# Kernel optimization log

Hardware: AMD Instinct MI355X
Metric: run time of the kernel (lower is better)

The kernel has to match this reference:

```python
import jax, jax.numpy as jnp
import numpy as np
import math

B, S, E, H = 4, 2048, 1024, 16
D = E // H
INFINITY = 1000000.0

def setup_inputs() -> dict:
    key = jax.random.key(0)
    ks = jax.random.split(key, 10)
    std = 1.0 / math.sqrt(E)
    inp = {
        "x": jax.random.normal(ks[0], (B, S, E), dtype=jnp.float32),
        "mask": jax.random.randint(ks[1], (B, S), 0, 2).astype(jnp.bool_),
        "WQ_w": jax.random.uniform(ks[2], (E, E), jnp.float32, -std, std),
        "WQ_b": jax.random.uniform(ks[3], (E,), jnp.float32, -std, std),
        "WK_w": jax.random.uniform(ks[4], (E, E), jnp.float32, -std, std),
        "WK_b": jax.random.uniform(ks[5], (E,), jnp.float32, -std, std),
        "WV_w": jax.random.uniform(ks[6], (E, E), jnp.float32, -std, std),
        "WV_b": jax.random.uniform(ks[7], (E,), jnp.float32, -std, std),
        "WO_w": jax.random.uniform(ks[8], (E, E), jnp.float32, -std, std),
        "WO_b": jax.random.uniform(ks[9], (E,), jnp.float32, -std, std),
    }
    return inp

def reference(x, mask, WQ_w, WQ_b, WK_w, WK_b, WV_w, WV_b, WO_w, WO_b):
    # Linear layers: y = x @ W.T + b (torch convention)
    q = (x @ WQ_w.T + WQ_b).reshape(B, S, H, D).transpose(0, 2, 1, 3)  # (B,H,S,D)
    k = (x @ WK_w.T + WK_b).reshape(B, S, H, D).transpose(0, 2, 1, 3)
    v = (x @ WV_w.T + WV_b).reshape(B, S, H, D).transpose(0, 2, 1, 3)
    score = jnp.einsum("bhqd,bhkd->bhqk", q, k) / math.sqrt(D)  # (B,H,S,S)
    # additive key mask: -infinity where mask is False
    inv_mask = (~mask).astype(jnp.float32)[:, None, None, :]  # (B,1,1,S)
    score = score - inv_mask * INFINITY
    attn = jax.nn.softmax(score, axis=-1)
    o = jnp.einsum("bhqk,bhkd->bhqd", attn, v)  # (B,H,S,D)
    o = o.transpose(0, 2, 1, 3).reshape(B, S, E)
    o = o @ WO_w.T + WO_b
    o = jnp.abs(o * mask.astype(jnp.float32)[:, :, None])
    return o
```

## Files before the change

### kernel.cpp

```cpp
#include <hip/hip_runtime.h>
#include <math.h>

#define B_ 4
#define S_ 2048
#define E_ 1024
#define H_ 16
#define D_ 64
#define MTOT (B_*S_)

typedef _Float16 half8v __attribute__((ext_vector_type(8)));
typedef _Float16 half4v __attribute__((ext_vector_type(4)));
typedef float f32x4 __attribute__((ext_vector_type(4)));
typedef float f32x16 __attribute__((ext_vector_type(16)));
typedef unsigned uint4v __attribute__((ext_vector_type(4)));

typedef __attribute__((address_space(1))) const void gconst_void;
typedef __attribute__((address_space(3))) void lds_void;

#define MFMA16(a,b,c) __builtin_amdgcn_mfma_f32_16x16x32_f16((a),(b),(c),0,0,0)
#define MFMA32(a,b,c) __builtin_amdgcn_mfma_f32_32x32x16_f16((a),(b),(c),0,0,0)

#define QSCALE 0.18033688011112042f

static __device__ __forceinline__ unsigned cvt_pk_u32(float a, float b) {
  return __builtin_bit_cast(unsigned, __builtin_amdgcn_cvt_pkrtz(a, b));
}

#if __has_builtin(__builtin_amdgcn_permlane32_swap)
static __device__ __forceinline__ void pl32_swap(unsigned a, unsigned b,
                                                 unsigned& rlo, unsigned& rhi) {
  auto r = __builtin_amdgcn_permlane32_swap(a, b, false, false);
  rlo = r[0]; rhi = r[1];
}
#else
static __device__ __forceinline__ void pl32_swap(unsigned a, unsigned b,
                                                 unsigned& rlo, unsigned& rhi) {
  const int hi = (threadIdx.x & 63) >> 5;
  unsigned t = __shfl_xor(hi ? a : b, 32);
  rlo = hi ? t : a;
  rhi = hi ? b : t;
}
#endif

static __device__ __forceinline__ float partner32(float v, int hi) {
  unsigned u = __builtin_bit_cast(unsigned, v);
  unsigned lo_, hi_;
  pl32_swap(u, u, lo_, hi_);
  return __builtin_bit_cast(float, hi ? lo_ : hi_);
}

__global__ __launch_bounds__(256) void cvt_w4(const float* __restrict__ w0, const float* __restrict__ w1,
                                              const float* __restrict__ w2, const float* __restrict__ w3,
                                              _Float16* __restrict__ o0, _Float16* __restrict__ o1,
                                              _Float16* __restrict__ o2, _Float16* __restrict__ o3) {
  const int z = blockIdx.y;
  const float* in = (z == 0) ? w0 : (z == 1) ? w1 : (z == 2) ? w2 : w3;
  _Float16* out = (z == 0) ? o0 : (z == 1) ? o1 : (z == 2) ? o2 : o3;
  int i = (blockIdx.x * 256 + threadIdx.x) * 4;
  float4 v = *(const float4*)(in + i);
  half4v o;
  o[0] = (_Float16)v.x; o[1] = (_Float16)v.y; o[2] = (_Float16)v.z; o[3] = (_Float16)v.w;
  *(half4v*)(out + i) = o;
}

__global__ __launch_bounds__(256) void zero_out(float* __restrict__ out) {
  const size_t i = ((size_t)blockIdx.x * 256 + threadIdx.x) * 4;
  float4 z = make_float4(0.f, 0.f, 0.f, 0.f);
  *(float4*)(out + i) = z;
}

__global__ __launch_bounds__(256) void mask_prep(const unsigned char* __restrict__ mraw,
                                                 _Float16* __restrict__ maskc,
                                                 float* __restrict__ qmask,
                                                 int* __restrict__ ks,
                                                 int* __restrict__ nkpa) {
  __shared__ int flags[2];
  __shared__ int psum[256];
  const int b = blockIdx.x, tid = threadIdx.x;
  if (tid < 2) flags[tid] = 1;
  __syncthreads();
  const unsigned int* w = (const unsigned int*)mraw;
  for (int i = tid; i < 2048; i += 256) {
    unsigned int v = w[i];
    if (!(v == 0u || v == 1u)) flags[0] = 0;
    if (!(v == 0u || v == 0x3f800000u)) flags[1] = 0;
  }
  __syncthreads();
  const int is_i32 = flags[0], is_f32 = flags[1];
  int m[8]; int cnt = 0;
  for (int i = 0; i < 8; ++i) {
    const int idx = b * 2048 + tid * 8 + i;
    int mv;
    if (is_i32)      mv = ((const int*)mraw)[idx];
    else if (is_f32) mv = (((const unsigned int*)mraw)[idx] != 0u);
    else             mv = (mraw[idx] != 0);
    m[i] = mv; cnt += mv;
    qmask[idx] = mv ? 1.0f : 0.0f;
  }
  psum[tid] = cnt;
  __syncthreads();
  for (int off = 1; off < 256; off <<= 1) {
    int u = (tid >= off) ? psum[tid - off] : 0;
    __syncthreads();
    psum[tid] += u;
    __syncthreads();
  }
  const int total = psum[255];
  int base = psum[tid] - cnt;
  for (int i = 0; i < 8; ++i)
    if (m[i]) ks[b * 2048 + (base++)] = tid * 8 + i;
  for (int j = tid; j < 2048; j += 256)
    maskc[b * 2048 + j] = (j < total) ? (_Float16)0.0f : (_Float16)(-60000.0f);
  __syncthreads();
  const int lastv = (total > 0) ? ks[b * 2048 + total - 1] : 0;
  for (int j = total + tid; j < 2048; j += 256)
    ks[b * 2048 + j] = lastv;
  if (tid == 0) nkpa[b] = (total + 127) & ~127;
}

__global__ __launch_bounds__(256) void cvt_xc(const float* __restrict__ x,
                                              const int* __restrict__ ks,
                                              const int* __restrict__ nkpa,
                                              _Float16* __restrict__ xc) {
  const int b = blockIdx.y, j = blockIdx.x;
  if (j >= nkpa[b]) return;
  const int s = ks[b * 2048 + j];
  const float* src = x + (size_t)(b * 2048 + s) * E_;
  _Float16* dst = xc + (size_t)(b * 2048 + j) * E_;
  const int i = threadIdx.x * 4;
  float4 v = *(const float4*)(src + i);
  half4v o;
  o[0] = (_Float16)v.x; o[1] = (_Float16)v.y; o[2] = (_Float16)v.z; o[3] = (_Float16)v.w;
  *(half4v*)(dst + i) = o;
}

template <int ROWS>
__device__ __forceinline__ void stageX64s(const _Float16* __restrict__ g, int ld,
                                          _Float16* lds, int wid, int lane) {
#pragma unroll
  for (int j = 0; j < ROWS / 32; ++j) {
    const int c = j * 256 + wid * 64 + lane;
    const int row = c >> 3, dslot = c & 7;
    const int sslot = dslot ^ (row & 7);
    const _Float16* src = g + (size_t)row * ld + sslot * 8;
    _Float16* dst = lds + (size_t)(j * 256 + wid * 64) * 8;
    __builtin_amdgcn_global_load_lds((gconst_void*)src, (lds_void*)dst, 16, 0, 0);
  }
}

__global__ __launch_bounds__(256) void qkv_gemm(
    const _Float16* __restrict__ xc, const int* __restrict__ nkpa,
    const _Float16* __restrict__ wq, const _Float16* __restrict__ wk, const _Float16* __restrict__ wv,
    const float* __restrict__ bq, const float* __restrict__ bkp, const float* __restrict__ bvp,
    _Float16* __restrict__ Qc, _Float16* __restrict__ Kc, _Float16* __restrict__ Vc) {
  const int id = blockIdx.x;
  const int tt = id / 96;
  const int rem = id % 96;
  const int bb = rem / 24;
  const int r2 = rem % 24;
  const int by = r2 / 3, z = r2 % 3;
  if (tt * 128 >= nkpa[bb]) return;
  __shared__ _Float16 As[128 * 64];
  __shared__ _Float16 Bs[128 * 64];
  const int tid = threadIdx.x, lane = tid & 63, wid = tid >> 6;
  const int g = lane >> 4, r16 = lane & 15;
  const int bm = (bb * 16 + tt) * 128, bn = by * 128;
  const _Float16* w = (z == 0) ? wq : (z == 1) ? wk : wv;
  const float* bias = (z == 0) ? bq : (z == 1) ? bkp : bvp;
  const int wr = wid >> 1, wc = wid & 1;
  const int sw = r16 & 7;
  f32x4 acc[4][4] = {};
  for (int k0 = 0; k0 < E_; k0 += 64) {
    stageX64s<128>(xc + (size_t)bm * E_ + k0, E_, As, wid, lane);
    stageX64s<128>(w + (size_t)bn * E_ + k0, E_, Bs, wid, lane);
    __syncthreads();
#pragma unroll
    for (int kk = 0; kk < 2; ++kk) {
      const int so = ((kk * 4 + g) ^ sw) * 8;
      half8v a[4], bf[4];
#pragma unroll
      for (int i = 0; i < 4; ++i) a[i] = *(const half8v*)&As[(wr * 64 + i * 16 + r16) * 64 + so];
#pragma unroll
      for (int j = 0; j < 4; ++j) bf[j] = *(const half8v*)&Bs[(wc * 64 + j * 16 + r16) * 64 + so];
#pragma unroll
      for (int i = 0; i < 4; ++i)
#pragma unroll
        for (int j = 0; j < 4; ++j) acc[i][j] = MFMA16(a[i], bf[j], acc[i][j]);
    }
    __syncthreads();
  }
#pragma unroll
  for (int i = 0; i < 4; ++i) {
#pragma unroll
    for (int j = 0; j < 4; ++j) {
      const int gn = bn + wc * 64 + j * 16 + r16;
      const float bb2 = bias[gn];
      const int h = gn >> 6, d = gn & 63;
      const int gm0 = bm + wr * 64 + i * 16 + g * 4;
      const int b_ = gm0 >> 11, s0 = gm0 & (S_ - 1);
      const size_t bhbase = (size_t)(b_ * H_ + h) * S_ * D_;
      if (z == 2) {
        half4v v4;
#pragma unroll
        for (int ii = 0; ii < 4; ++ii) v4[ii] = (_Float16)(acc[i][j][ii] + bb2);
        *(half4v*)&Vc[bhbase + (size_t)(s0 >> 4) * (D_ * 16) + d * 16 + (s0 & 15)] = v4;
      } else if (z == 1) {
#pragma unroll
        for (int ii = 0; ii < 4; ++ii) {
          const int s = s0 + ii;
          Kc[bhbase + (size_t)(s >> 5) * 2048 + (d >> 4) * 512 + (s & 31) * 16 + (d & 15)] =
              (_Float16)(acc[i][j][ii] + bb2);
        }
      } else {
#pragma unroll
        for (int ii = 0; ii < 4; ++ii)
          Qc[bhbase + (size_t)(s0 + ii) * D_ + d] = (_Float16)((acc[i][j][ii] + bb2) * QSCALE);
      }
    }
  }
}

__global__ __launch_bounds__(512) void attn_kernel(
    const _Float16* __restrict__ Qc, const _Float16* __restrict__ Kc, const _Float16* __restrict__ Vc,
    const _Float16* __restrict__ maskc, const int* __restrict__ nkpa,
    _Float16* __restrict__ Oc) {
  __shared__ float mlds[4][64][36];
  _Float16* smask = (_Float16*)&mlds[0][0][0];
  const int tid = threadIdx.x, lane = tid & 63, wid = tid >> 6;
  const int c = lane & 31, hi = lane >> 5;
  const int qg = wid & 3, kh = wid >> 2;
  const int id = blockIdx.x;
  const int slot = id & 7, hbh = (id >> 3) & 7, t = id >> 6;
  const int hb = hbh * 8 + slot;
  const int b = hb >> 4, h = hb & 15;
  const int nkp = nkpa[b];
  if (t * 128 >= nkp) return;
  const size_t bh = (size_t)(b * H_ + h);
  const _Float16* Qb = Qc + bh * S_ * D_;
  const _Float16* Kb = Kc + bh * S_ * D_;
  const _Float16* Vb = Vc + bh * S_ * D_;

  *((half4v*)smask + tid) = *((const half4v*)(maskc + (size_t)b * S_) + tid);

  const int jq = t * 128 + qg * 32 + c;

  half8v qb[4];
#pragma unroll
  for (int kc = 0; kc < 4; ++kc)
    qb[kc] = *(const half8v*)&Qb[(size_t)jq * D_ + 16 * kc + 8 * hi];

  half8v bone = {};
  if (hi == 0) bone[0] = (_Float16)1.0f;
  const f32x16 fzero = {};

  f32x16 oacc[2] = {};
  float mrun = -1e30f, lrun = 0.f;
  const int laneoff = c * 16 + 8 * hi;
  const int nkh = nkp >> 1;
  const int kb0 = kh * nkh;

  __syncthreads();

  half8v kaf[4];
  {
    const _Float16* ktb = Kb + (size_t)(kb0 >> 5) * 2048 + laneoff;
#pragma unroll
    for (int kc = 0; kc < 4; ++kc) kaf[kc] = *(const half8v*)&ktb[kc * 512];
  }
  _Float16 mv = smask[kb0 + c];

  for (int kb = kb0; kb < kb0 + nkh; kb += 32) {
    half8v amask = {};
    if (hi == 0) amask[0] = mv;
    __builtin_amdgcn_s_setprio(1);
    f32x16 sc = MFMA32(amask, bone, fzero);
    sc = MFMA32(kaf[0], qb[0], sc);
    sc = MFMA32(kaf[1], qb[1], sc);
    sc = MFMA32(kaf[2], qb[2], sc);
    sc = MFMA32(kaf[3], qb[3], sc);
    __builtin_amdgcn_s_setprio(0);
    const int kbn = (kb + 32 < kb0 + nkh) ? kb + 32 : kb0;
    {
      const _Float16* ktb = Kb + (size_t)(kbn >> 5) * 2048 + laneoff;
#pragma unroll
      for (int kc = 0; kc < 4; ++kc) kaf[kc] = *(const half8v*)&ktb[kc * 512];
    }
    mv = smask[kbn + c];
    const _Float16* v_base = Vb + (size_t)(kb >> 4) * (D_ * 16) + laneoff;
    half8v va00 = *(const half8v*)&v_base[0];
    half8v va01 = *(const half8v*)&v_base[512];
    half8v va10 = *(const half8v*)&v_base[1024];
    half8v va11 = *(const half8v*)&v_base[1024 + 512];
    float t0 = fmaxf(sc[0], sc[4]), t1 = fmaxf(sc[1], sc[5]);
    float t2 = fmaxf(sc[2], sc[6]), t3 = fmaxf(sc[3], sc[7]);
    t0 = fmaxf(fmaxf(sc[8], sc[12]), t0);
    t1 = fmaxf(fmaxf(sc[9], sc[13]), t1);
    t2 = fmaxf(fmaxf(sc[10], sc[14]), t2);
    t3 = fmaxf(fmaxf(sc[11], sc[15]), t3);
    float pmax = fmaxf(fmaxf(t0, t1), fmaxf(t2, t3));
    pmax = fmaxf(pmax, partner32(pmax, hi));
    if (__any(pmax > mrun + 11.0f)) {
      float mnew = fmaxf(mrun, pmax);
      float corr = __builtin_amdgcn_exp2f(mrun - mnew);
      mrun = mnew;
      lrun *= corr;
#pragma unroll
      for (int dt = 0; dt < 2; ++dt)
#pragma unroll
        for (int r = 0; r < 16; ++r) oacc[dt][r] *= corr;
    }
    float ps0 = 0.f, ps1 = 0.f;
#pragma unroll
    for (int sl = 0; sl < 2; ++sl) {
      const int bs = 8 * sl;
      float p0 = __builtin_amdgcn_exp2f(sc[bs + 0] - mrun);
      float p1 = __builtin_amdgcn_exp2f(sc[bs + 1] - mrun);
      float p2 = __builtin_amdgcn_exp2f(sc[bs + 2] - mrun);
      float p3 = __builtin_amdgcn_exp2f(sc[bs + 3] - mrun);
      float p4 = __builtin_amdgcn_exp2f(sc[bs + 4] - mrun);
      float p5 = __builtin_amdgcn_exp2f(sc[bs + 5] - mrun);
      float p6 = __builtin_amdgcn_exp2f(sc[bs + 6] - mrun);
      float p7 = __builtin_amdgcn_exp2f(sc[bs + 7] - mrun);
      ps0 += (p0 + p1) + (p2 + p3);
      ps1 += (p4 + p5) + (p6 + p7);
      unsigned uA = cvt_pk_u32(p0, p1);
      unsigned uB = cvt_pk_u32(p2, p3);
      unsigned uC = cvt_pk_u32(p4, p5);
      unsigned uD = cvt_pk_u32(p6, p7);
      unsigned w0, w1, w2, w3;
      pl32_swap(uA, uC, w0, w2);
      pl32_swap(uB, uD, w1, w3);
      uint4v u4 = {w0, w1, w2, w3};
      half8v pb = __builtin_bit_cast(half8v, u4);
      __builtin_amdgcn_s_setprio(1);
      oacc[0] = MFMA32(sl ? va10 : va00, pb, oacc[0]);
      oacc[1] = MFMA32(sl ? va11 : va01, pb, oacc[1]);
      __builtin_amdgcn_s_setprio(0);
    }
    lrun += ps0 + ps1;
  }
  lrun += partner32(lrun, hi);
  __syncthreads();
  if (kh == 1) {
    float* p = &mlds[qg][lane][0];
#pragma unroll
    for (int dt = 0; dt < 2; ++dt)
#pragma unroll
      for (int rr = 0; rr < 4; ++rr) {
        float4 v4 = make_float4(oacc[dt][4 * rr], oacc[dt][4 * rr + 1],
                                oacc[dt][4 * rr + 2], oacc[dt][4 * rr + 3]);
        *(float4*)&p[dt * 16 + rr * 4] = v4;
      }
    p[32] = mrun;
    p[33] = lrun;
  }
  __syncthreads();
  if (kh == 0) {
    const float* p = &mlds[qg][lane][0];
    const float mB = p[32], lB = p[33];
    const float mS = fmaxf(mrun, mB);
    const float cA = __builtin_amdgcn_exp2f(mrun - mS);
    const float cB = __builtin_amdgcn_exp2f(mB - mS);
    const float inv = 1.0f / (lrun * cA + lB * cB);
    const float fA = cA * inv, fB = cB * inv;
    _Float16* orow = Oc + ((size_t)(b * S_ + jq)) * E_ + h * D_;
#pragma unroll
    for (int dt = 0; dt < 2; ++dt)
#pragma unroll
      for (int rr = 0; rr < 4; ++rr) {
        float4 vB = *(const float4*)&p[dt * 16 + rr * 4];
        half4v o4;
        o4[0] = (_Float16)(oacc[dt][4 * rr + 0] * fA + vB.x * fB);
        o4[1] = (_Float16)(oacc[dt][4 * rr + 1] * fA + vB.y * fB);
        o4[2] = (_Float16)(oacc[dt][4 * rr + 2] * fA + vB.z * fB);
        o4[3] = (_Float16)(oacc[dt][4 * rr + 3] * fA + vB.w * fB);
        *(half4v*)&orow[32 * dt + 8 * rr + 4 * hi] = o4;
      }
  }
}

__global__ __launch_bounds__(256) void oproj_gemm(
    const _Float16* __restrict__ Oc, const _Float16* __restrict__ wo, const float* __restrict__ bo,
    const int* __restrict__ ks, const int* __restrict__ nkpa, float* __restrict__ out) {
  const int id = blockIdx.x;
  const int jt = id / 32;
  const int rem = id % 32;
  const int bb = rem / 8, by = rem % 8;
  if (jt * 64 >= nkpa[bb]) return;
  __shared__ _Float16 As[64 * 64];
  __shared__ _Float16 Bs[128 * 64];
  const int tid = threadIdx.x, lane = tid & 63, wid = tid >> 6;
  const int g = lane >> 4, r16 = lane & 15;
  const int bm = bb * 2048 + jt * 64, bn = by * 128;
  const int wr = wid >> 1, wc = wid & 1;
  const int sw = r16 & 7;
  f32x4 acc[2][4] = {};
  for (int k0 = 0; k0 < E_; k0 += 64) {
    stageX64s<64>(Oc + (size_t)bm * E_ + k0, E_, As, wid, lane);
    stageX64s<128>(wo + (size_t)bn * E_ + k0, E_, Bs, wid, lane);
    __syncthreads();
#pragma unroll
    for (int kk = 0; kk < 2; ++kk) {
      const int so = ((kk * 4 + g) ^ sw) * 8;
      half8v a[2], bf[4];
#pragma unroll
      for (int i = 0; i < 2; ++i) a[i] = *(const half8v*)&As[(wr * 32 + i * 16 + r16) * 64 + so];
#pragma unroll
      for (int j = 0; j < 4; ++j) bf[j] = *(const half8v*)&Bs[(wc * 64 + j * 16 + r16) * 64 + so];
#pragma unroll
      for (int i = 0; i < 2; ++i)
#pragma unroll
        for (int j = 0; j < 4; ++j) acc[i][j] = MFMA16(a[i], bf[j], acc[i][j]);
    }
    __syncthreads();
  }
#pragma unroll
  for (int i = 0; i < 2; ++i) {
#pragma unroll
    for (int j = 0; j < 4; ++j) {
      const int gn = bn + wc * 64 + j * 16 + r16;
      const float bb2 = bo[gn];
      const int gm0 = bm + wr * 32 + i * 16 + g * 4;
#pragma unroll
      for (int ii = 0; ii < 4; ++ii) {
        const int gm = gm0 + ii;
        const int b_ = gm >> 11, j_ = gm & (S_ - 1);
        const int sorig = ks[b_ * 2048 + j_];
        const float y = acc[i][j][ii] + bb2;
        out[((size_t)(b_ * S_ + sorig)) * E_ + gn] = fabsf(y);
      }
    }
  }
}

extern "C" void kernel_launch(void* const* d_in, const int* in_sizes, int n_in,
                              void* d_out, int out_size, void* d_ws, size_t ws_size,
                              hipStream_t stream) {
  const float* x = (const float*)d_in[0];
  const unsigned char* mask = (const unsigned char*)d_in[1];
  const float* WQ_w = (const float*)d_in[2];
  const float* WQ_b = (const float*)d_in[3];
  const float* WK_w = (const float*)d_in[4];
  const float* WK_b = (const float*)d_in[5];
  const float* WV_w = (const float*)d_in[6];
  const float* WV_b = (const float*)d_in[7];
  const float* WO_w = (const float*)d_in[8];
  const float* WO_b = (const float*)d_in[9];

  char* ws = (char*)d_ws;
  size_t off = 0;
  _Float16* xc  = (_Float16*)(ws + off); off += (size_t)MTOT * E_ * 2;
  _Float16* wqh = (_Float16*)(ws + off); off += (size_t)E_ * E_ * 2;
  _Float16* wkh = (_Float16*)(ws + off); off += (size_t)E_ * E_ * 2;
  _Float16* wvh = (_Float16*)(ws + off); off += (size_t)E_ * E_ * 2;
  _Float16* woh = (_Float16*)(ws + off); off += (size_t)E_ * E_ * 2;
  _Float16* Qc  = (_Float16*)(ws + off); off += (size_t)MTOT * E_ * 2;
  _Float16* Kc  = (_Float16*)(ws + off); off += (size_t)MTOT * E_ * 2;
  _Float16* Vc  = (_Float16*)(ws + off); off += (size_t)MTOT * E_ * 2;
  _Float16* Oc  = (_Float16*)(ws + off); off += (size_t)MTOT * E_ * 2;
  _Float16* maskcf = (_Float16*)(ws + off); off += (size_t)B_ * S_ * 2;
  float* qmaskf = (float*)(ws + off); off += (size_t)B_ * S_ * 4;
  int* ksl      = (int*)(ws + off); off += (size_t)B_ * S_ * 4;
  int* nkpa     = (int*)(ws + off); off += 64;
  if (ws_size < off) return;

  const int NW = E_ * E_;
  mask_prep<<<dim3(B_), dim3(256), 0, stream>>>(mask, maskcf, qmaskf, ksl, nkpa);
  cvt_w4<<<dim3(NW / 4 / 256, 4), dim3(256), 0, stream>>>(WQ_w, WK_w, WV_w, WO_w,
                                                          wqh, wkh, wvh, woh);
  cvt_xc<<<dim3(S_, B_), dim3(256), 0, stream>>>(x, ksl, nkpa, xc);
  zero_out<<<dim3(MTOT * E_ / 4 / 256), dim3(256), 0, stream>>>((float*)d_out);
  qkv_gemm<<<dim3(1536), dim3(256), 0, stream>>>(
      xc, nkpa, wqh, wkh, wvh, WQ_b, WK_b, WV_b, Qc, Kc, Vc);
  attn_kernel<<<dim3((S_ / 128) * H_ * B_), dim3(512), 0, stream>>>(
      Qc, Kc, Vc, maskcf, nkpa, Oc);
  oproj_gemm<<<dim3(32 * 32), dim3(256), 0, stream>>>(Oc, woh, WO_b, ksl, nkpa, (float*)d_out);
}
```

Baseline: 136.2 us.

## Double-buffer LDS staging in QKV and output projection GEMMs

Both projection GEMMs now keep two LDS buffers per operand. Each iteration issues the async global-to-LDS loads for the next K tile before computing on the current one, so one barrier per iteration replaces two. The aim is to overlap global memory latency with MFMA work. In exchange, LDS use per block doubles, which may lower occupancy, and correctness depends on the async LDS loads being complete by the trailing barrier.

Result: no change. 134.8 us (-1.0%).

```diff
diff --git a/kernel.cpp b/kernel.cpp
--- a/kernel.cpp
+++ b/kernel.cpp
@@ -160,8 +160,8 @@
   const int r2 = rem % 24;
   const int by = r2 / 3, z = r2 % 3;
   if (tt * 128 >= nkpa[bb]) return;
-  __shared__ _Float16 As[128 * 64];
-  __shared__ _Float16 Bs[128 * 64];
+  __shared__ _Float16 As[2][128 * 64];
+  __shared__ _Float16 Bs[2][128 * 64];
   const int tid = threadIdx.x, lane = tid & 63, wid = tid >> 6;
   const int g = lane >> 4, r16 = lane & 15;
   const int bm = (bb * 16 + tt) * 128, bn = by * 128;
@@ -170,24 +170,33 @@
   const int wr = wid >> 1, wc = wid & 1;
   const int sw = r16 & 7;
   f32x4 acc[4][4] = {};
+  stageX64s<128>(xc + (size_t)bm * E_, E_, As[0], wid, lane);
+  stageX64s<128>(w + (size_t)bn * E_, E_, Bs[0], wid, lane);
+  __syncthreads();
+  int cur = 0;
   for (int k0 = 0; k0 < E_; k0 += 64) {
-    stageX64s<128>(xc + (size_t)bm * E_ + k0, E_, As, wid, lane);
-    stageX64s<128>(w + (size_t)bn * E_ + k0, E_, Bs, wid, lane);
-    __syncthreads();
+    const int kn = k0 + 64;
+    if (kn < E_) {
+      stageX64s<128>(xc + (size_t)bm * E_ + kn, E_, As[cur ^ 1], wid, lane);
+      stageX64s<128>(w + (size_t)bn * E_ + kn, E_, Bs[cur ^ 1], wid, lane);
+    }
+    const _Float16* Ac = As[cur];
+    const _Float16* Bc = Bs[cur];
 #pragma unroll
     for (int kk = 0; kk < 2; ++kk) {
       const int so = ((kk * 4 + g) ^ sw) * 8;
       half8v a[4], bf[4];
 #pragma unroll
-      for (int i = 0; i < 4; ++i) a[i] = *(const half8v*)&As[(wr * 64 + i * 16 + r16) * 64 + so];
-#pragma unroll
-      for (int j = 0; j < 4; ++j) bf[j] = *(const half8v*)&Bs[(wc * 64 + j * 16 + r16) * 64 + so];
+      for (int i = 0; i < 4; ++i) a[i] = *(const half8v*)&Ac[(wr * 64 + i * 16 + r16) * 64 + so];
+#pragma unroll
+      for (int j = 0; j < 4; ++j) bf[j] = *(const half8v*)&Bc[(wc * 64 + j * 16 + r16) * 64 + so];
 #pragma unroll
       for (int i = 0; i < 4; ++i)
 #pragma unroll
         for (int j = 0; j < 4; ++j) acc[i][j] = MFMA16(a[i], bf[j], acc[i][j]);
     }
     __syncthreads();
+    cur ^= 1;
   }
 #pragma unroll
   for (int i = 0; i < 4; ++i) {
@@ -387,32 +396,41 @@
   const int rem = id % 32;
   const int bb = rem / 8, by = rem % 8;
   if (jt * 64 >= nkpa[bb]) return;
-  __shared__ _Float16 As[64 * 64];
-  __shared__ _Float16 Bs[128 * 64];
+  __shared__ _Float16 As[2][64 * 64];
+  __shared__ _Float16 Bs[2][128 * 64];
   const int tid = threadIdx.x, lane = tid & 63, wid = tid >> 6;
   const int g = lane >> 4, r16 = lane & 15;
   const int bm = bb * 2048 + jt * 64, bn = by * 128;
   const int wr = wid >> 1, wc = wid & 1;
   const int sw = r16 & 7;
   f32x4 acc[2][4] = {};
+  stageX64s<64>(Oc + (size_t)bm * E_, E_, As[0], wid, lane);
+  stageX64s<128>(wo + (size_t)bn * E_, E_, Bs[0], wid, lane);
+  __syncthreads();
+  int cur = 0;
   for (int k0 = 0; k0 < E_; k0 += 64) {
-    stageX64s<64>(Oc + (size_t)bm * E_ + k0, E_, As, wid, lane);
-    stageX64s<128>(wo + (size_t)bn * E_ + k0, E_, Bs, wid, lane);
-    __syncthreads();
+    const int kn = k0 + 64;
+    if (kn < E_) {
+      stageX64s<64>(Oc + (size_t)bm * E_ + kn, E_, As[cur ^ 1], wid, lane);
+      stageX64s<128>(wo + (size_t)bn * E_ + kn, E_, Bs[cur ^ 1], wid, lane);
+    }
+    const _Float16* Ac = As[cur];
+    const _Float16* Bc = Bs[cur];
 #pragma unroll
     for (int kk = 0; kk < 2; ++kk) {
       const int so = ((kk * 4 + g) ^ sw) * 8;
       half8v a[2], bf[4];
 #pragma unroll
-      for (int i = 0; i < 2; ++i) a[i] = *(const half8v*)&As[(wr * 32 + i * 16 + r16) * 64 + so];
-#pragma unroll
-      for (int j = 0; j < 4; ++j) bf[j] = *(const half8v*)&Bs[(wc * 64 + j * 16 + r16) * 64 + so];
+      for (int i = 0; i < 2; ++i) a[i] = *(const half8v*)&Ac[(wr * 32 + i * 16 + r16) * 64 + so];
+#pragma unroll
+      for (int j = 0; j < 4; ++j) bf[j] = *(const half8v*)&Bc[(wc * 64 + j * 16 + r16) * 64 + so];
 #pragma unroll
       for (int i = 0; i < 2; ++i)
 #pragma unroll
         for (int j = 0; j < 4; ++j) acc[i][j] = MFMA16(a[i], bf[j], acc[i][j]);
     }
     __syncthreads();
+    cur ^= 1;
   }
 #pragma unroll
   for (int i = 0; i < 2; ++i) {
```
